# Performance work log

Hardware: AMD Instinct MI355X
Metric: run time of the kernel (lower is better)

Reference implementation:

```python
import jax, jax.numpy as jnp
import numpy as np

N = 50000        # n_nodes
E = 1_600_000    # n_edges (avg degree 32)
IN = 128         # in_dim
H = 8            # num_heads
R = 16           # hidden_rank
D = 16           # out_dim (per head)
SCALE = float(np.sqrt(D))


def setup_inputs() -> dict:
    key = jax.random.key(0)
    k1, k2, k3, k4, k5, k6 = jax.random.split(key, 6)
    h = jax.random.normal(k1, (N, IN), jnp.float32)
    src = jax.random.randint(k2, (E,), 0, N, dtype=jnp.int32)
    dst = jax.random.randint(k3, (E,), 0, N, dtype=jnp.int32)
    s = 1.0 / np.sqrt(IN)  # kaiming-ish scale
    p = jax.random.normal(k4, (IN, H * R), jnp.float32) * s
    q = jax.random.normal(k5, (IN, H * R), jnp.float32) * s
    Wv = jax.random.normal(k6, (IN, H * D), jnp.float32) * s
    return {"h": h, "src": src, "dst": dst, "p": p, "q": q, "Wv": Wv}


def reference(h, src, dst, p, q, Wv):
    # global_attention_type == 'transform' -> atted = h
    K = (h @ q).reshape(N, H, R)   # K_h = atted @ _q
    Q = (h @ p).reshape(N, H, R)   # Q_h = h @ _p
    V = (h @ Wv).reshape(N, H, D)  # V_h = V(h), no bias
    # per-edge score: (K[src] * Q[dst]).sum(-1, keepdim), then scaled exp
    score = jnp.sum(K[src] * Q[dst], axis=-1, keepdims=True)   # [E, H, 1]
    score = jnp.exp(jnp.clip(score / SCALE, -5.0, 5.0))
    # scatter-sum into destination nodes
    wV = jax.ops.segment_sum(V[src] * score, dst, num_segments=N)  # [N, H, D]
    z = jax.ops.segment_sum(score, dst, num_segments=N)            # [N, H, 1]
    z = jnp.where(z == 0, jnp.float32(0.001), z)
    return wV / z
```

## Files before the change

### kernel.cpp

```cpp
#include <hip/hip_runtime.h>
#include <hip/hip_fp16.h>


#define HNODE 64
#define EPB   4096
#define BKT_SHIFT 7
#define BKT_CAP 5120
#define CHUNK 40

typedef _Float16 f16x8 __attribute__((ext_vector_type(8)));
typedef float    f32x4 __attribute__((ext_vector_type(4)));
typedef _Float16 hv2   __attribute__((ext_vector_type(2)));

__device__ __forceinline__ float fdot2(unsigned a, unsigned b, float c) {
#if __has_builtin(__builtin_amdgcn_fdot2)
    return __builtin_amdgcn_fdot2(__builtin_bit_cast(hv2, a),
                                  __builtin_bit_cast(hv2, b), c, false);
#else
    __half2 ah = *(__half2*)&a, bh = *(__half2*)&b;
    float2 af = __half22float2(ah), bf = __half22float2(bh);
    return c + af.x * bf.x + af.y * bf.y;
#endif
}

__device__ __forceinline__ float2 h2f(unsigned u) {
    __half2 hh = *(__half2*)&u;
    return __half22float2(hh);
}

__device__ __forceinline__ unsigned pack2(float a, float b) {
    __half2 hh = __floats2half2_rn(a, b);
    return *(unsigned*)&hh;
}

__global__ __launch_bounds__(256) void wt_convert_kernel(
    const float* __restrict__ Wq, const float* __restrict__ Wp,
    const float* __restrict__ Wv, __half* __restrict__ Wt)
{
    int o = blockIdx.x * 256 + threadIdx.x;
    int m = o >> 14, rem = o & 16383;
    int nn = rem >> 7, kk = rem & 127;
    const float* W = (m == 0) ? Wq : (m == 1) ? Wp : Wv;
    Wt[o] = __float2half(W[kk * 128 + nn]);
}

__global__ __launch_bounds__(256) void gemm_scatter_kernel(
    const float* __restrict__ h, const __half* __restrict__ Wt,
    unsigned* __restrict__ KV, __half* __restrict__ Q, int n,
    const int* __restrict__ src, const int* __restrict__ dst,
    unsigned* __restrict__ ebuf, int* __restrict__ cnts,
    int E, int nbkt, int nblk_e, int gemm_blocks)
{
    __shared__ __align__(16) char smem[39936];
    const int t = threadIdx.x;

    if ((int)blockIdx.x < gemm_blocks) {
        _Float16* ws = (_Float16*)smem;
        const int wid = t >> 6, lane = t & 63;
        const int node0 = blockIdx.x * HNODE;
        const int mrow = lane & 15, quad = lane >> 4;

        const int row = node0 + wid * 16 + mrow;
        const bool rowvalid = (row < n);
        const int rowc = rowvalid ? row : (n - 1);

        f16x8 hfr[4];
        #pragma unroll
        for (int s = 0; s < 4; s++) {
            const float4* hp = (const float4*)(h + (size_t)rowc * 128 + quad * 8 + 32 * s);
            float4 f0 = hp[0], f1 = hp[1];
            f16x8 a;
            a[0] = (_Float16)f0.x; a[1] = (_Float16)f0.y;
            a[2] = (_Float16)f0.z; a[3] = (_Float16)f0.w;
            a[4] = (_Float16)f1.x; a[5] = (_Float16)f1.y;
            a[6] = (_Float16)f1.z; a[7] = (_Float16)f1.w;
            hfr[s] = a;
        }

        f32x4 acc[3][8];
        #pragma unroll
        for (int m = 0; m < 3; m++)
            #pragma unroll
            for (int ct = 0; ct < 8; ct++) acc[m][ct] = (f32x4){0.f, 0.f, 0.f, 0.f};

        #pragma unroll
        for (int m = 0; m < 3; m++) {
            __syncthreads();
            {
                const uint4* wg = (const uint4*)(Wt + (size_t)m * 16384);
                #pragma unroll
                for (int i = 0; i < 8; i++) {
                    int idx = t * 8 + i;
                    int r = idx >> 4, seg = idx & 15;
                    *(uint4*)(ws + r * 136 + seg * 8) = wg[idx];
                }
            }
            __syncthreads();
            #pragma unroll
            for (int s = 0; s < 4; s++) {
                #pragma unroll
                for (int ct = 0; ct < 8; ct++) {
                    f16x8 a = *(const f16x8*)(ws + (ct * 16 + mrow) * 136 + quad * 8 + 32 * s);
                    acc[m][ct] = __builtin_amdgcn_mfma_f32_16x16x32_f16(a, hfr[s], acc[m][ct], 0, 0, 0);
                }
            }
        }

        if (rowvalid) {
            unsigned* kvrow = KV + (size_t)row * 128;
            __half*   qrow  = Q  + (size_t)row * 128;
            #pragma unroll
            for (int ct = 0; ct < 8; ct++) {
                int qd = ct * 4 + quad;
                uint4 ov;
                ov.x = pack2(acc[0][ct][0], acc[0][ct][1]);
                ov.y = pack2(acc[0][ct][2], acc[0][ct][3]);
                ov.z = pack2(acc[2][ct][0], acc[2][ct][1]);
                ov.w = pack2(acc[2][ct][2], acc[2][ct][3]);
                *(uint4*)(kvrow + 4 * qd) = ov;
                uint2 qv;
                qv.x = pack2(acc[1][ct][0], acc[1][ct][1]);
                qv.y = pack2(acc[1][ct][2], acc[1][ct][3]);
                *(uint2*)(qrow + 4 * qd) = qv;
            }
        }
    } else {
        unsigned long long* sorted = (unsigned long long*)smem;
        int* cnt  = (int*)(smem + 32768);
        int* lofs = (int*)(smem + 34816);
        int* ts   = (int*)(smem + 36864);
        int* tot_sh = (int*)(smem + 37888);

        int blk = blockIdx.x - gemm_blocks;
        for (int i = t; i < 512; i += 256) cnt[i] = 0;
        __syncthreads();

        int4 sv[4], dv[4], rk[4];
        int base = blk * EPB + t * 4;
        #pragma unroll
        for (int r = 0; r < 4; r++) {
            int i = base + r * 1024;
            if (i + 3 < E) {
                sv[r] = *(const int4*)(src + i);
                dv[r] = *(const int4*)(dst + i);
            } else {
                int tsrc[4], tdst[4];
                for (int k = 0; k < 4; k++) {
                    int j = i + k;
                    tsrc[k] = (j < E) ? src[j] : 0;
                    tdst[k] = (j < E) ? dst[j] : -1;
                }
                sv[r] = make_int4(tsrc[0], tsrc[1], tsrc[2], tsrc[3]);
                dv[r] = make_int4(tdst[0], tdst[1], tdst[2], tdst[3]);
            }
            rk[r].x = (dv[r].x >= 0) ? atomicAdd(&cnt[dv[r].x >> BKT_SHIFT], 1) : 0;
            rk[r].y = (dv[r].y >= 0) ? atomicAdd(&cnt[dv[r].y >> BKT_SHIFT], 1) : 0;
            rk[r].z = (dv[r].z >= 0) ? atomicAdd(&cnt[dv[r].z >> BKT_SHIFT], 1) : 0;
            rk[r].w = (dv[r].w >= 0) ? atomicAdd(&cnt[dv[r].w >> BKT_SHIFT], 1) : 0;
        }
        __syncthreads();

        for (int i = t; i < nbkt; i += 256)
            cnts[blk * 512 + i] = cnt[i];

        int c0 = cnt[2 * t], c1 = cnt[2 * t + 1];
        int ps = c0 + c1;
        ts[t] = ps; __syncthreads();
        for (int off = 1; off < 256; off <<= 1) {
            int x = ts[t];
            int y = (t >= off) ? ts[t - off] : 0;
            __syncthreads();
            ts[t] = x + y;
            __syncthreads();
        }
        int pbase = ts[t] - ps;
        lofs[2 * t] = pbase;
        lofs[2 * t + 1] = pbase + c0;
        if (t == 255) *tot_sh = ts[255];
        __syncthreads();

        #pragma unroll
        for (int r = 0; r < 4; r++) {
            int s, d;
            d = dv[r].x; if (d >= 0) { s = sv[r].x; sorted[lofs[d >> BKT_SHIFT] + rk[r].x] = ((unsigned long long)d << 18) | (unsigned)s; }
            d = dv[r].y; if (d >= 0) { s = sv[r].y; sorted[lofs[d >> BKT_SHIFT] + rk[r].y] = ((unsigned long long)d << 18) | (unsigned)s; }
            d = dv[r].z; if (d >= 0) { s = sv[r].z; sorted[lofs[d >> BKT_SHIFT] + rk[r].z] = ((unsigned long long)d << 18) | (unsigned)s; }
            d = dv[r].w; if (d >= 0) { s = sv[r].w; sorted[lofs[d >> BKT_SHIFT] + rk[r].w] = ((unsigned long long)d << 18) | (unsigned)s; }
        }
        __syncthreads();

        int tot = *tot_sh;
        #pragma unroll
        for (int j = 0; j < 16; j++) {
            int i = j * 256 + t;
            if (i < tot) {
                unsigned long long e = sorted[i];
                int d = (int)(e >> 18);
                int b = d >> BKT_SHIFT;
                int k = i - lofs[b];
                if (k < CHUNK)
                    ebuf[((size_t)b * nblk_e + blk) * CHUNK + k] =
                        ((unsigned)(d & 127) << 18) | (unsigned)(e & 0x3FFFFu);
            }
        }
    }
}

__global__ __launch_bounds__(512) void fine_scatter_kernel(
    const unsigned* __restrict__ ebuf, const int* __restrict__ cnts,
    int2* __restrict__ offs, int* __restrict__ csr, int N, int nblk_e, int nbkt)
{
    __shared__ int cval[512];
    __shared__ int cofs[512];
    __shared__ int ts[512];
    __shared__ int ldeg[128];
    __shared__ int lstart[129];
    __shared__ int tot_sh;
    __shared__ unsigned sedge[BKT_CAP];
    __shared__ unsigned short srank[BKT_CAP];
    __shared__ int lcsr[BKT_CAP];

    int b = blockIdx.x, t = threadIdx.x;
    int node_base = b << BKT_SHIFT;
    int seg0 = b * BKT_CAP;

    int c = (t < nblk_e) ? cnts[t * 512 + b] : 0;
    if (c > CHUNK) c = CHUNK;
    cval[t] = c;
    ts[t] = c;
    if (t < 128) ldeg[t] = 0;
    __syncthreads();
    for (int off = 1; off < 512; off <<= 1) {
        int x = ts[t];
        int y = (t >= off) ? ts[t - off] : 0;
        __syncthreads();
        ts[t] = x + y;
        __syncthreads();
    }
    cofs[t] = ts[t] - cval[t];
    if (t == 511) tot_sh = (ts[511] <= BKT_CAP) ? ts[511] : BKT_CAP;
    __syncthreads();

    for (int idx = t; idx < nblk_e * CHUNK; idx += 512) {
        int cc = idx / CHUNK, k = idx - cc * CHUNK;
        if (k < cval[cc]) {
            int pos = cofs[cc] + k;
            if (pos < BKT_CAP)
                sedge[pos] = ebuf[((size_t)b * nblk_e + cc) * CHUNK + k];
        }
    }
    __syncthreads();

    int tot = tot_sh;
    for (int i = t; i < tot; i += 512)
        srank[i] = (unsigned short)atomicAdd(&ldeg[sedge[i] >> 18], 1);
    __syncthreads();

    int mydeg = (t < 128) ? ldeg[t] : 0;
    if (t < 128) ts[t] = mydeg;
    __syncthreads();
    for (int off = 1; off < 128; off <<= 1) {
        int x = (t < 128) ? ts[t] : 0;
        int y = (t >= off && t < 128) ? ts[t - off] : 0;
        __syncthreads();
        if (t < 128) ts[t] = x + y;
        __syncthreads();
    }
    if (t < 128) {
        int lbeg = ts[t] - mydeg;
        lstart[t] = lbeg;
        int node = node_base + t;
        if (node < N) offs[node] = make_int2(seg0 + lbeg, seg0 + lbeg + mydeg);
    }
    if (t == 127) lstart[128] = ts[127];
    __syncthreads();

    for (int i = t; i < tot; i += 512) {
        unsigned v = sedge[i];
        lcsr[lstart[v >> 18] + srank[i]] = (int)(v & 0x3FFFFu);
    }
    __syncthreads();

    for (int i = t; i < tot; i += 512)
        csr[seg0 + i] = lcsr[i];
}

__global__ __launch_bounds__(256) void aggregate_kernel(
    const uint4* __restrict__ KV, const uint2* __restrict__ Qr,
    const int2* __restrict__ offs, const int* __restrict__ csr,
    float4* __restrict__ out, int n)
{
    int t = threadIdx.x;
    int node = blockIdx.x * 4 + (t >> 6);
    if (node >= n) return;
    int lane = t & 63;
    int l = lane & 31;
    int eh = lane >> 5;

    uint2 qq = Qr[(size_t)node * 32 + l];
    int2 be = offs[node];
    int beg = be.x, cnt = be.y - be.x;

    float4 accV = make_float4(0.f, 0.f, 0.f, 0.f);
    float accZ = 0.f;

    int chunkbase = 0;
    int myidx = (beg + lane < be.y) ? csr[beg + lane] : 0;

    uint4 kvA = make_uint4(0, 0, 0, 0), kvB = make_uint4(0, 0, 0, 0);
    if (cnt > 0) kvA = KV[(size_t)__shfl(myidx, eh, 64) * 32 + l];
    if (cnt > 2) kvB = KV[(size_t)__shfl(myidx, 2 + eh, 64) * 32 + l];

    for (int e = 0; e < cnt; e += 2) {
        uint4 nkv;
        bool more = (e + 4 < cnt);
        if (more) {
            int off = e + 4 - chunkbase;
            if (off == 64) {
                chunkbase += 64;
                myidx = (beg + chunkbase + lane < be.y) ? csr[beg + chunkbase + lane] : 0;
                off = 0;
            }
            nkv = KV[(size_t)__shfl(myidx, off + eh, 64) * 32 + l];
        }
        float p = fdot2(kvA.x, qq.x, fdot2(kvA.y, qq.y, 0.f));
        p += __shfl_xor(p, 1);
        p += __shfl_xor(p, 2);
        float x = fminf(fmaxf(p * 0.25f, -5.f), 5.f);
        float sc = (e + eh < cnt) ? __expf(x) : 0.f;
        accZ += sc;
        float2 va = h2f(kvA.z), vb = h2f(kvA.w);
        accV.x += sc * va.x; accV.y += sc * va.y;
        accV.z += sc * vb.x; accV.w += sc * vb.y;
        kvA = kvB;
        if (more) kvB = nkv;
    }

    accZ   += __shfl_xor(accZ, 32);
    accV.x += __shfl_xor(accV.x, 32);
    accV.y += __shfl_xor(accV.y, 32);
    accV.z += __shfl_xor(accV.z, 32);
    accV.w += __shfl_xor(accV.w, 32);

    if (lane < 32) {
        if (accZ == 0.f) accZ = 0.001f;
        float inv = 1.0f / accZ;
        out[(size_t)node * 32 + l] =
            make_float4(accV.x * inv, accV.y * inv, accV.z * inv, accV.w * inv);
    }
}


extern "C" void kernel_launch(void* const* d_in, const int* in_sizes, int n_in,
                              void* d_out, int out_size, void* d_ws, size_t ws_size,
                              hipStream_t stream)
{
    const float* h   = (const float*)d_in[0];
    const int*   src = (const int*)d_in[1];
    const int*   dst = (const int*)d_in[2];
    const float* p   = (const float*)d_in[3];
    const float* q   = (const float*)d_in[4];
    const float* wv  = (const float*)d_in[5];
    float* out = (float*)d_out;

    const int N = in_sizes[0] / 128;
    const int E = in_sizes[1];
    const int nbkt = (N + 127) >> BKT_SHIFT;
    const int nblk_e = (E + EPB - 1) / EPB;
    const int gemm_blocks = (N + HNODE - 1) / HNODE;

    unsigned* KV = (unsigned*)d_ws;
    __half* Qh   = (__half*)(KV + (size_t)N * 128);
    unsigned* ebuf = (unsigned*)(Qh + (size_t)N * 128);
    int* cnts    = (int*)(ebuf + (size_t)nbkt * nblk_e * CHUNK);
    int* csr     = cnts + (size_t)nblk_e * 512;
    int2* offs   = (int2*)(csr + (size_t)nbkt * BKT_CAP);
    __half* Wt   = (__half*)(offs + N);

    wt_convert_kernel<<<192, 256, 0, stream>>>(q, p, wv, Wt);

    gemm_scatter_kernel<<<gemm_blocks + nblk_e, 256, 0, stream>>>(
        h, Wt, KV, Qh, N, src, dst, ebuf, cnts, E, nbkt, nblk_e, gemm_blocks);

    fine_scatter_kernel<<<nbkt, 512, 0, stream>>>(ebuf, cnts, offs, csr, N, nblk_e, nbkt);

    aggregate_kernel<<<(N + 3) / 4, 256, 0, stream>>>(
        (const uint4*)KV, (const uint2*)Qh, offs, csr, (float4*)out, N);
}
```

Measured before the change: 244.4 us.

## Split GEMM per weight matrix and pack scatter keys into 32 bits

Each GEMM block now computes a single projection (K, Q or V), so the launch has three times as many GEMM blocks. Each holds only one weight tile and one accumulator set instead of looping over three with extra barriers, and the h rows are re-read three times. Edge-sort blocks are scheduled first. Sorted edge keys are packed as 32-bit (dst<<16|src) instead of 64-bit, which halves the shared memory used by sorting and raises possible occupancy. This packing assumes node indices fit in 16 bits.

```diff
diff --git a/kernel.cpp b/kernel.cpp
--- a/kernel.cpp
+++ b/kernel.cpp
@@ -49,16 +49,29 @@
     unsigned* __restrict__ KV, __half* __restrict__ Q, int n,
     const int* __restrict__ src, const int* __restrict__ dst,
     unsigned* __restrict__ ebuf, int* __restrict__ cnts,
-    int E, int nbkt, int nblk_e, int gemm_blocks)
-{
-    __shared__ __align__(16) char smem[39936];
+    int E, int nbkt, int nblk_e)
+{
+    __shared__ __align__(16) char smem[34816];
     const int t = threadIdx.x;
 
-    if ((int)blockIdx.x < gemm_blocks) {
+    if ((int)blockIdx.x >= nblk_e) {
         _Float16* ws = (_Float16*)smem;
+        const int gblk = blockIdx.x - nblk_e;
+        const int m = gblk % 3;
+        const int tile = gblk / 3;
         const int wid = t >> 6, lane = t & 63;
-        const int node0 = blockIdx.x * HNODE;
+        const int node0 = tile * HNODE;
         const int mrow = lane & 15, quad = lane >> 4;
+
+        {
+            const uint4* wg = (const uint4*)(Wt + (size_t)m * 16384);
+            #pragma unroll
+            for (int i = 0; i < 8; i++) {
+                int idx = t * 8 + i;
+                int r = idx >> 4, seg = idx & 15;
+                *(uint4*)(ws + r * 136 + seg * 8) = wg[idx];
+            }
+        }
 
         const int row = node0 + wid * 16 + mrow;
         const bool rowvalid = (row < n);
@@ -77,62 +90,41 @@
             hfr[s] = a;
         }
 
-        f32x4 acc[3][8];
-        #pragma unroll
-        for (int m = 0; m < 3; m++)
+        f32x4 acc[8];
+        #pragma unroll
+        for (int ct = 0; ct < 8; ct++) acc[ct] = (f32x4){0.f, 0.f, 0.f, 0.f};
+
+        __syncthreads();
+        #pragma unroll
+        for (int s = 0; s < 4; s++) {
             #pragma unroll
-            for (int ct = 0; ct < 8; ct++) acc[m][ct] = (f32x4){0.f, 0.f, 0.f, 0.f};
-
-        #pragma unroll
-        for (int m = 0; m < 3; m++) {
-            __syncthreads();
-            {
-                const uint4* wg = (const uint4*)(Wt + (size_t)m * 16384);
-                #pragma unroll
-                for (int i = 0; i < 8; i++) {
-                    int idx = t * 8 + i;
-                    int r = idx >> 4, seg = idx & 15;
-                    *(uint4*)(ws + r * 136 + seg * 8) = wg[idx];
-                }
-            }
-            __syncthreads();
-            #pragma unroll
-            for (int s = 0; s < 4; s++) {
-                #pragma unroll
-                for (int ct = 0; ct < 8; ct++) {
-                    f16x8 a = *(const f16x8*)(ws + (ct * 16 + mrow) * 136 + quad * 8 + 32 * s);
-                    acc[m][ct] = __builtin_amdgcn_mfma_f32_16x16x32_f16(a, hfr[s], acc[m][ct], 0, 0, 0);
-                }
+            for (int ct = 0; ct < 8; ct++) {
+                f16x8 a = *(const f16x8*)(ws + (ct * 16 + mrow) * 136 + quad * 8 + 32 * s);
+                acc[ct] = __builtin_amdgcn_mfma_f32_16x16x32_f16(a, hfr[s], acc[ct], 0, 0, 0);
             }
         }
 
         if (rowvalid) {
-            unsigned* kvrow = KV + (size_t)row * 128;
-            __half*   qrow  = Q  + (size_t)row * 128;
             #pragma unroll
             for (int ct = 0; ct < 8; ct++) {
                 int qd = ct * 4 + quad;
-                uint4 ov;
-                ov.x = pack2(acc[0][ct][0], acc[0][ct][1]);
-                ov.y = pack2(acc[0][ct][2], acc[0][ct][3]);
-                ov.z = pack2(acc[2][ct][0], acc[2][ct][1]);
-                ov.w = pack2(acc[2][ct][2], acc[2][ct][3]);
-                *(uint4*)(kvrow + 4 * qd) = ov;
-                uint2 qv;
-                qv.x = pack2(acc[1][ct][0], acc[1][ct][1]);
-                qv.y = pack2(acc[1][ct][2], acc[1][ct][3]);
-                *(uint2*)(qrow + 4 * qd) = qv;
+                uint2 v;
+                v.x = pack2(acc[ct][0], acc[ct][1]);
+                v.y = pack2(acc[ct][2], acc[ct][3]);
+                if (m == 0)      *(uint2*)(KV + (size_t)row * 128 + 4 * qd) = v;
+                else if (m == 2) *(uint2*)(KV + (size_t)row * 128 + 4 * qd + 2) = v;
+                else             *(uint2*)(Q  + (size_t)row * 128 + 4 * qd) = v;
             }
         }
     } else {
-        unsigned long long* sorted = (unsigned long long*)smem;
-        int* cnt  = (int*)(smem + 32768);
-        int* lofs = (int*)(smem + 34816);
-        int* ts   = (int*)(smem + 36864);
-        int* tot_sh = (int*)(smem + 37888);
-
-        int blk = blockIdx.x - gemm_blocks;
-        for (int i = t; i < 512; i += 256) cnt[i] = 0;
+        unsigned* sorted = (unsigned*)smem;
+        int* cnt    = (int*)(smem + 16384);
+        int* lofs   = (int*)(smem + 20480);
+        int* ts     = (int*)(smem + 24576);
+        int* tot_sh = (int*)(smem + 25600);
+
+        int blk = blockIdx.x;
+        for (int i = t; i < 1024; i += 256) cnt[i] = 0;
         __syncthreads();
 
         int4 sv[4], dv[4], rk[4];
@@ -161,10 +153,10 @@
         __syncthreads();
 
         for (int i = t; i < nbkt; i += 256)
-            cnts[blk * 512 + i] = cnt[i];
-
-        int c0 = cnt[2 * t], c1 = cnt[2 * t + 1];
-        int ps = c0 + c1;
+            cnts[blk * 1024 + i] = cnt[i];
+
+        int c0 = cnt[4 * t], c1 = cnt[4 * t + 1], c2 = cnt[4 * t + 2], c3 = cnt[4 * t + 3];
+        int ps = c0 + c1 + c2 + c3;
         ts[t] = ps; __syncthreads();
         for (int off = 1; off < 256; off <<= 1) {
             int x = ts[t];
@@ -173,19 +165,21 @@
             ts[t] = x + y;
             __syncthreads();
         }
-        int pbase = ts[t] - ps;
-        lofs[2 * t] = pbase;
-        lofs[2 * t + 1] = pbase + c0;
+        int pb = ts[t] - ps;
+        lofs[4 * t] = pb;
+        lofs[4 * t + 1] = pb + c0;
+        lofs[4 * t + 2] = pb + c0 + c1;
+        lofs[4 * t + 3] = pb + c0 + c1 + c2;
         if (t == 255) *tot_sh = ts[255];
         __syncthreads();
 
         #pragma unroll
         for (int r = 0; r < 4; r++) {
             int s, d;
-            d = dv[r].x; if (d >= 0) { s = sv[r].x; sorted[lofs[d >> BKT_SHIFT] + rk[r].x] = ((unsigned long long)d << 18) | (unsigned)s; }
-            d = dv[r].y; if (d >= 0) { s = sv[r].y; sorted[lofs[d >> BKT_SHIFT] + rk[r].y] = ((unsigned long long)d << 18) | (unsigned)s; }
-            d = dv[r].z; if (d >= 0) { s = sv[r].z; sorted[lofs[d >> BKT_SHIFT] + rk[r].z] = ((unsigned long long)d << 18) | (unsigned)s; }
-            d = dv[r].w; if (d >= 0) { s = sv[r].w; sorted[lofs[d >> BKT_SHIFT] + rk[r].w] = ((unsigned long long)d << 18) | (unsigned)s; }
+            d = dv[r].x; if (d >= 0) { s = sv[r].x; sorted[lofs[d >> BKT_SHIFT] + rk[r].x] = ((unsigned)d << 16) | (unsigned)s; }
+            d = dv[r].y; if (d >= 0) { s = sv[r].y; sorted[lofs[d >> BKT_SHIFT] + rk[r].y] = ((unsigned)d << 16) | (unsigned)s; }
+            d = dv[r].z; if (d >= 0) { s = sv[r].z; sorted[lofs[d >> BKT_SHIFT] + rk[r].z] = ((unsigned)d << 16) | (unsigned)s; }
+            d = dv[r].w; if (d >= 0) { s = sv[r].w; sorted[lofs[d >> BKT_SHIFT] + rk[r].w] = ((unsigned)d << 16) | (unsigned)s; }
         }
         __syncthreads();
 
@@ -194,13 +188,11 @@
         for (int j = 0; j < 16; j++) {
             int i = j * 256 + t;
             if (i < tot) {
-                unsigned long long e = sorted[i];
-                int d = (int)(e >> 18);
-                int b = d >> BKT_SHIFT;
+                unsigned e = sorted[i];
+                int b = (int)(e >> (16 + BKT_SHIFT));
                 int k = i - lofs[b];
                 if (k < CHUNK)
-                    ebuf[((size_t)b * nblk_e + blk) * CHUNK + k] =
-                        ((unsigned)(d & 127) << 18) | (unsigned)(e & 0x3FFFFu);
+                    ebuf[((size_t)b * nblk_e + blk) * CHUNK + k] = e & 0x7FFFFFu;
             }
         }
     }
@@ -224,7 +216,7 @@
     int node_base = b << BKT_SHIFT;
     int seg0 = b * BKT_CAP;
 
-    int c = (t < nblk_e) ? cnts[t * 512 + b] : 0;
+    int c = (t < nblk_e) ? cnts[(size_t)t * 1024 + b] : 0;
     if (c > CHUNK) c = CHUNK;
     cval[t] = c;
     ts[t] = c;
@@ -253,7 +245,7 @@
 
     int tot = tot_sh;
     for (int i = t; i < tot; i += 512)
-        srank[i] = (unsigned short)atomicAdd(&ldeg[sedge[i] >> 18], 1);
+        srank[i] = (unsigned short)atomicAdd(&ldeg[sedge[i] >> 16], 1);
     __syncthreads();
 
     int mydeg = (t < 128) ? ldeg[t] : 0;
@@ -277,7 +269,7 @@
 
     for (int i = t; i < tot; i += 512) {
         unsigned v = sedge[i];
-        lcsr[lstart[v >> 18] + srank[i]] = (int)(v & 0x3FFFFu);
+        lcsr[lstart[v >> 16] + srank[i]] = (int)(v & 0xFFFFu);
     }
     __syncthreads();
 
@@ -367,20 +359,20 @@
     const int E = in_sizes[1];
     const int nbkt = (N + 127) >> BKT_SHIFT;
     const int nblk_e = (E + EPB - 1) / EPB;
-    const int gemm_blocks = (N + HNODE - 1) / HNODE;
+    const int ntile = (N + HNODE - 1) / HNODE;
 
     unsigned* KV = (unsigned*)d_ws;
     __half* Qh   = (__half*)(KV + (size_t)N * 128);
     unsigned* ebuf = (unsigned*)(Qh + (size_t)N * 128);
     int* cnts    = (int*)(ebuf + (size_t)nbkt * nblk_e * CHUNK);
-    int* csr     = cnts + (size_t)nblk_e * 512;
+    int* csr     = cnts + (size_t)nblk_e * 1024;
     int2* offs   = (int2*)(csr + (size_t)nbkt * BKT_CAP);
     __half* Wt   = (__half*)(offs + N);
 
     wt_convert_kernel<<<192, 256, 0, stream>>>(q, p, wv, Wt);
 
-    gemm_scatter_kernel<<<gemm_blocks + nblk_e, 256, 0, stream>>>(
-        h, Wt, KV, Qh, N, src, dst, ebuf, cnts, E, nbkt, nblk_e, gemm_blocks);
+    gemm_scatter_kernel<<<nblk_e + 3 * ntile, 256, 0, stream>>>(
+        h, Wt, KV, Qh, N, src, dst, ebuf, cnts, E, nbkt, nblk_e);
 
     fine_scatter_kernel<<<nbkt, 512, 0, stream>>>(ebuf, cnts, offs, csr, N, nblk_e, nbkt);
 
```

New measurement: 246.2 us. Within noise of the previous version (+0.8%).
